# Kernel tuning notes

Measured on AMD Instinct MI355X. Metric: run time of the kernel, lower is better.

The kernel has to match this reference:

```python
import jax, jax.numpy as jnp
import numpy as np

G, KS = 8, 3          # groups, kernel size
K = KS * KS           # sampling points per group
OM = 32               # per-group offset_mask dim: ceil(3K/8)*8
EPS = 1e-5


def setup_inputs() -> dict:
    key = jax.random.key(0)
    ks = jax.random.split(key, 12)
    N, C, H, W = 4, 128, 64, 64
    x = jax.random.normal(ks[0], (N, C, H, W), jnp.float32)
    w_value = jax.random.normal(ks[1], (C, C), jnp.float32) / np.sqrt(C)
    b_value = jax.random.normal(ks[2], (C,), jnp.float32) * 0.01
    # small offset weights -> modest sampling offsets (real module inits these to 0)
    w_off = jax.random.normal(ks[3], (C, G * OM), jnp.float32) * 0.02
    b_off = jax.random.normal(ks[4], (G * OM,), jnp.float32) * 0.01
    w_out = jax.random.normal(ks[5], (C, C), jnp.float32) / np.sqrt(C)
    b_out = jax.random.normal(ks[6], (C,), jnp.float32) * 0.01
    bn_gamma = jax.random.uniform(ks[7], (C,), jnp.float32, 0.5, 1.5)
    bn_beta = jax.random.normal(ks[8], (C,), jnp.float32) * 0.1
    bn_mean = jax.random.normal(ks[9], (C,), jnp.float32) * 0.1
    bn_var = jax.random.uniform(ks[10], (C,), jnp.float32, 0.5, 1.5)
    return dict(x=x, w_value=w_value, b_value=b_value, w_off=w_off, b_off=b_off,
                w_out=w_out, b_out=b_out, bn_gamma=bn_gamma, bn_beta=bn_beta,
                bn_mean=bn_mean, bn_var=bn_var)


def _dcnv4(x, w_value, b_value, w_off, b_off, w_out, b_out,
           bn_gamma, bn_beta, bn_mean, bn_var):
    N, C, H, W = x.shape
    Cg = C // G
    P = H * W
    xf = x.transpose(0, 2, 3, 1).reshape(N, P, C)              # N,P,C (channels-last tokens)
    val = xf @ w_value + b_value                               # value projection
    om = (xf @ w_off + b_off).reshape(N, P, G, OM)             # offsets+mask (padded to 32)
    offset = om[..., :2 * K].reshape(N, P, G, K, 2)            # (dx, dy) pairs
    mask = om[..., 2 * K:3 * K]                                # modulation, NO softmax (DCNv4)

    # base sampling grid: output pixel + centered 3x3 footprint (stride 1, dil 1)
    py, px = jnp.meshgrid(jnp.arange(H), jnp.arange(W), indexing='ij')
    kk = jnp.arange(KS) - (KS - 1) // 2
    ky, kx = jnp.meshgrid(kk, kk, indexing='ij')
    base_y = (py.reshape(-1)[:, None] + ky.reshape(-1)[None, :]).astype(x.dtype)  # P,K
    base_x = (px.reshape(-1)[:, None] + kx.reshape(-1)[None, :]).astype(x.dtype)
    sy = base_y[None, :, None, :] + offset[..., 1]             # N,P,G,K sampling y
    sx = base_x[None, :, None, :] + offset[..., 0]             # N,P,G,K sampling x

    vflat = val.reshape(N, P, G, Cg).transpose(0, 2, 1, 3)     # N,G,P,Cg

    def gather(iy, ix):
        lin = jnp.clip(iy, 0, H - 1) * W + jnp.clip(ix, 0, W - 1)   # N,P,G,K
        lin = lin.transpose(0, 2, 1, 3).reshape(N, G, P * K)
        g = jnp.take_along_axis(vflat, lin[..., None], axis=2)      # N,G,P*K,Cg
        return g.reshape(N, G, P, K, Cg).transpose(0, 2, 1, 3, 4)   # N,P,G,K,Cg

    y0 = jnp.floor(sy); x0 = jnp.floor(sx)
    ty = sy - y0; tx = sx - x0
    y0i = y0.astype(jnp.int32); x0i = x0.astype(jnp.int32)

    def valid(iy, ix):
        return ((iy >= 0) & (iy < H) & (ix >= 0) & (ix < W)).astype(x.dtype)

    acc = jnp.zeros((N, P, G, K, Cg), x.dtype)
    for dy, dx, wgt in ((0, 0, (1 - ty) * (1 - tx)), (0, 1, (1 - ty) * tx),
                        (1, 0, ty * (1 - tx)), (1, 1, ty * tx)):
        iy, ix = y0i + dy, x0i + dx
        acc = acc + gather(iy, ix) * (wgt * valid(iy, ix))[..., None]

    out = (acc * mask[..., None]).sum(axis=3)                  # aggregate over K -> N,P,G,Cg
    out = out.reshape(N, P, C) @ w_out + b_out                 # output projection
    out = out.reshape(N, H, W, C).transpose(0, 3, 1, 2)        # back to NCHW

    # BatchNorm (inference) + SiLU
    inv = bn_gamma / jnp.sqrt(bn_var + EPS)
    out = out * inv[None, :, None, None] + (bn_beta - bn_mean * inv)[None, :, None, None]
    return out * jax.nn.sigmoid(out)


def reference(x, w_value, b_value, w_off, b_off, w_out, b_out,
              bn_gamma, bn_beta, bn_mean, bn_var):
    return _dcnv4(x, w_value, b_value, w_off, b_off, w_out, b_out,
                  bn_gamma, bn_beta, bn_mean, bn_var)
```

## Files before the change

### kernel.cpp

```cpp
#include <hip/hip_runtime.h>
#include <cstdint>

typedef __bf16 v8bf __attribute__((ext_vector_type(8)));
typedef float f32x4 __attribute__((ext_vector_type(4)));

#define BN_EPS 1e-5f

__device__ __forceinline__ float b2f(uint32_t u) {
    union { uint32_t i; float f; } v; v.i = u << 16; return v.f;
}
__device__ __forceinline__ uint16_t f2b(float f) {
    uint32_t u = __builtin_bit_cast(uint32_t, f);
    u += 0x7fffu + ((u >> 16) & 1u);
    return (uint16_t)(u >> 16);
}

__global__ void prep_transpose_kernel(const float* __restrict__ x,
                                      const float* __restrict__ wv, const float* __restrict__ wo,
                                      const float* __restrict__ wout,
                                      const float* __restrict__ gamma, const float* __restrict__ beta,
                                      const float* __restrict__ mean, const float* __restrict__ var,
                                      uint16_t* __restrict__ xf, uint16_t* __restrict__ wT,
                                      float* __restrict__ bnc) {
    int bid = blockIdx.x;
    if (bid < 512) {
        __shared__ float lds[64 * 65];
        int cb = bid & 1, pb = (bid >> 1) & 63, n = bid >> 7;
        int c0 = cb * 64, p0 = pb * 64;
        int l = threadIdx.x & 63, q = threadIdx.x >> 6;
        const float* xp = x + ((size_t)(n * 128 + c0)) * 4096 + p0;
#pragma unroll
        for (int i = 0; i < 16; i++) {
            int c = i * 4 + q;
            lds[l * 65 + c] = xp[(size_t)c * 4096 + l];
        }
        __syncthreads();
#pragma unroll
        for (int i = 0; i < 16; i++) {
            int pr = i * 4 + q;
            xf[((size_t)(n * 4096 + p0 + pr)) * 128 + c0 + l] = f2b(lds[pr * 65 + l]);
        }
    } else {
        int idx = (bid - 512) * 256 + threadIdx.x;
        if (idx < 512 * 128) {
            int r = idx >> 7, ci = idx & 127;
            float v;
            if (r < 128)      v = wv[ci * 128 + r];
            else if (r < 384) v = wo[ci * 256 + (r - 128)];
            else              v = wout[ci * 128 + (r - 384)];
            wT[idx] = f2b(v);
        }
        if (idx < 128) {
            float inv = gamma[idx] * rsqrtf(var[idx] + BN_EPS);
            bnc[idx] = inv;
            bnc[128 + idx] = beta[idx] - mean[idx] * inv;
        }
    }
}

__launch_bounds__(256)
__global__ void gemm1_kernel(const uint16_t* __restrict__ xf, const uint16_t* __restrict__ wT,
                             const float* __restrict__ b_value, const float* __restrict__ b_off,
                             uint16_t* __restrict__ valb, uint16_t* __restrict__ omb) {
    __shared__ __align__(16) uint16_t ldsX[128 * 136];
    __shared__ __align__(16) uint16_t ldsW[64 * 136];
    int ct = blockIdx.x;
    int pt = blockIdx.y;
    int p0 = pt * 128, cbase = ct * 64;
    int tid = threadIdx.x;
    int col16 = tid & 15, rowq = tid >> 4;

    const uint4* xg = (const uint4*)xf;
    uint4* lx = (uint4*)ldsX;
#pragma unroll
    for (int i = 0; i < 8; i++) {
        int row = i * 16 + rowq;
        lx[row * 17 + col16] = xg[(size_t)(p0 + row) * 16 + col16];
    }
    const uint4* wg = (const uint4*)wT;
    uint4* lw = (uint4*)ldsW;
#pragma unroll
    for (int i = 0; i < 4; i++) {
        int row = i * 16 + rowq;
        lw[row * 17 + col16] = wg[(size_t)(cbase + row) * 16 + col16];
    }
    __syncthreads();

    int wv = tid >> 6, lane = tid & 63;
    int ln = lane & 15, quad = lane >> 4;
    int cW = cbase + wv * 16 + quad * 4;
    f32x4 binit;
    if (cW < 128) binit = f32x4{b_value[cW], b_value[cW + 1], b_value[cW + 2], b_value[cW + 3]};
    else          binit = f32x4{b_off[cW - 128], b_off[cW - 127], b_off[cW - 126], b_off[cW - 125]};
    f32x4 acc[8];
#pragma unroll
    for (int t = 0; t < 8; t++) acc[t] = binit;

#pragma unroll
    for (int kk = 0; kk < 4; kk++) {
        v8bf a = *(const v8bf*)&ldsW[(wv * 16 + ln) * 136 + kk * 32 + quad * 8];
#pragma unroll
        for (int t = 0; t < 8; t++) {
            v8bf b = *(const v8bf*)&ldsX[(t * 16 + ln) * 136 + kk * 32 + quad * 8];
            acc[t] = __builtin_amdgcn_mfma_f32_16x16x32_bf16(a, b, acc[t], 0, 0, 0);
        }
    }

    int nimg = p0 >> 12, pin0 = p0 & 4095;
    if (cW < 128) {
        int g = cW >> 4, cg = cW & 15;
#pragma unroll
        for (int t = 0; t < 8; t++) {
            int p = pin0 + t * 16 + ln;
            uint32_t u0 = (uint32_t)f2b(acc[t][0]) | ((uint32_t)f2b(acc[t][1]) << 16);
            uint32_t u1 = (uint32_t)f2b(acc[t][2]) | ((uint32_t)f2b(acc[t][3]) << 16);
            *(uint2*)&valb[(((size_t)(nimg * 8 + g) * 4096 + p) << 4) + cg] = make_uint2(u0, u1);
        }
    } else {
        int j0 = cW - 128;
#pragma unroll
        for (int t = 0; t < 8; t++) {
            int p = pin0 + t * 16 + ln;
            uint32_t u0 = (uint32_t)f2b(acc[t][0]) | ((uint32_t)f2b(acc[t][1]) << 16);
            uint32_t u1 = (uint32_t)f2b(acc[t][2]) | ((uint32_t)f2b(acc[t][3]) << 16);
            *(uint2*)&omb[((size_t)(nimg * 4096 + p) << 8) + j0] = make_uint2(u0, u1);
        }
    }
}

__launch_bounds__(256)
__global__ void gather_gemm3_kernel(const uint16_t* __restrict__ omb, const uint16_t* __restrict__ valb,
                                    const uint16_t* __restrict__ wT,
                                    const float* __restrict__ b_out, const float* __restrict__ bnc,
                                    float* __restrict__ out) {
    __shared__ __align__(16) uint16_t ldsA[64 * 136];
    __shared__ __align__(16) uint16_t ldsW[128 * 136];
    int pt = blockIdx.x;
    int p0 = pt * 64;
    int n = p0 >> 12, pin0 = p0 & 4095;
    int tid = threadIdx.x;

    {
        int col16 = tid & 15, rowq = tid >> 4;
        const uint4* wg = (const uint4*)wT;
        uint4* lw = (uint4*)ldsW;
#pragma unroll
        for (int i = 0; i < 8; i++) {
            int row = i * 16 + rowq;
            lw[row * 17 + col16] = wg[(size_t)(384 + row) * 16 + col16];
        }
    }

    int g = tid >> 5, pl = tid & 31;
    const uint4* vb = (const uint4*)(valb + ((size_t)(n * 8 + g) << 16));
#pragma unroll
    for (int pp = 0; pp < 2; pp++) {
        int prow = pp * 32 + pl;
        int p = p0 + prow;
        int pin = p & 4095;
        int py = pin >> 6, px = pin & 63;

        const uint16_t* op = omb + ((size_t)p << 8) + g * 32;
        uint4 q0 = *(const uint4*)(op);
        uint4 q1 = *(const uint4*)(op + 8);
        uint4 q2 = *(const uint4*)(op + 16);
        uint2 q3 = *(const uint2*)(op + 24);
        uint32_t w[14] = {q0.x, q0.y, q0.z, q0.w, q1.x, q1.y, q1.z, q1.w,
                          q2.x, q2.y, q2.z, q2.w, q3.x, q3.y};
        float o[28];
#pragma unroll
        for (int i = 0; i < 14; i++) { o[2 * i] = b2f(w[i] & 0xffff); o[2 * i + 1] = b2f(w[i] >> 16); }

        float acc[16];
#pragma unroll
        for (int i = 0; i < 16; i++) acc[i] = 0.f;

#pragma unroll
        for (int k = 0; k < 9; k++) {
            float sx = (float)(px + (k % 3) - 1) + o[2 * k];
            float sy = (float)(py + (k / 3) - 1) + o[2 * k + 1];
            float m = o[18 + k];
            float x0f = floorf(sx), y0f = floorf(sy);
            float tx = sx - x0f, ty = sy - y0f;
            int x0 = (int)x0f, y0 = (int)y0f;
#pragma unroll
            for (int dy = 0; dy < 2; dy++) {
                int iy = y0 + dy;
                if (iy < 0 || iy > 63) continue;
                float wy = dy ? ty : 1.f - ty;
#pragma unroll
                for (int dx = 0; dx < 2; dx++) {
                    int ix = x0 + dx;
                    if (ix < 0 || ix > 63) continue;
                    float wgt = m * wy * (dx ? tx : 1.f - tx);
                    const uint4* vp = vb + ((size_t)(iy * 64 + ix)) * 2;
                    uint4 v0 = vp[0], v1 = vp[1];
                    acc[0]  += wgt * b2f(v0.x & 0xffff); acc[1]  += wgt * b2f(v0.x >> 16);
                    acc[2]  += wgt * b2f(v0.y & 0xffff); acc[3]  += wgt * b2f(v0.y >> 16);
                    acc[4]  += wgt * b2f(v0.z & 0xffff); acc[5]  += wgt * b2f(v0.z >> 16);
                    acc[6]  += wgt * b2f(v0.w & 0xffff); acc[7]  += wgt * b2f(v0.w >> 16);
                    acc[8]  += wgt * b2f(v1.x & 0xffff); acc[9]  += wgt * b2f(v1.x >> 16);
                    acc[10] += wgt * b2f(v1.y & 0xffff); acc[11] += wgt * b2f(v1.y >> 16);
                    acc[12] += wgt * b2f(v1.z & 0xffff); acc[13] += wgt * b2f(v1.z >> 16);
                    acc[14] += wgt * b2f(v1.w & 0xffff); acc[15] += wgt * b2f(v1.w >> 16);
                }
            }
        }
        uint32_t u[8];
#pragma unroll
        for (int i = 0; i < 8; i++)
            u[i] = (uint32_t)f2b(acc[2 * i]) | ((uint32_t)f2b(acc[2 * i + 1]) << 16);
        uint4* outp = (uint4*)&ldsA[prow * 136 + g * 16];
        outp[0] = make_uint4(u[0], u[1], u[2], u[3]);
        outp[1] = make_uint4(u[4], u[5], u[6], u[7]);
    }
    __syncthreads();

    int wv = tid >> 6, lane = tid & 63;
    int ln = lane & 15, quad = lane >> 4;
    f32x4 acc[8];
#pragma unroll
    for (int ni = 0; ni < 8; ni++) {
        float b = b_out[ni * 16 + ln];
        acc[ni] = f32x4{b, b, b, b};
    }
#pragma unroll
    for (int kk = 0; kk < 4; kk++) {
        v8bf a = *(const v8bf*)&ldsA[(wv * 16 + ln) * 136 + kk * 32 + quad * 8];
#pragma unroll
        for (int ni = 0; ni < 8; ni++) {
            v8bf b = *(const v8bf*)&ldsW[(ni * 16 + ln) * 136 + kk * 32 + quad * 8];
            acc[ni] = __builtin_amdgcn_mfma_f32_16x16x32_bf16(a, b, acc[ni], 0, 0, 0);
        }
    }
    int p = pin0 + wv * 16 + quad * 4;
#pragma unroll
    for (int ni = 0; ni < 8; ni++) {
        int cc = ni * 16 + ln;
        float inv = bnc[cc], add = bnc[128 + cc];
        float4 r;
        float* rp = &r.x;
#pragma unroll
        for (int q = 0; q < 4; q++) {
            float z = acc[ni][q] * inv + add;
            rp[q] = z / (1.f + __expf(-z));
        }
        *(float4*)&out[((size_t)(n * 128 + cc) << 12) + p] = r;
    }
}

extern "C" void kernel_launch(void* const* d_in, const int* in_sizes, int n_in,
                              void* d_out, int out_size, void* d_ws, size_t ws_size,
                              hipStream_t stream) {
    const float* x       = (const float*)d_in[0];
    const float* w_value = (const float*)d_in[1];
    const float* b_value = (const float*)d_in[2];
    const float* w_off   = (const float*)d_in[3];
    const float* b_off   = (const float*)d_in[4];
    const float* w_out   = (const float*)d_in[5];
    const float* b_out   = (const float*)d_in[6];
    const float* gamma   = (const float*)d_in[7];
    const float* beta    = (const float*)d_in[8];
    const float* mean    = (const float*)d_in[9];
    const float* var     = (const float*)d_in[10];
    float* out = (float*)d_out;

    char* ws = (char*)d_ws;
    uint16_t* xf   = (uint16_t*)(ws);
    uint16_t* valb = (uint16_t*)(ws + ((size_t)8 << 20));
    uint16_t* omb  = (uint16_t*)(ws + ((size_t)12 << 20));
    uint16_t* wT   = (uint16_t*)(ws + ((size_t)20 << 20));
    float*    bnc  = (float*)(ws + ((size_t)20 << 20) + (1 << 18));

    hipLaunchKernelGGL(prep_transpose_kernel, dim3(768), dim3(256), 0, stream,
                       x, w_value, w_off, w_out, gamma, beta, mean, var, xf, wT, bnc);
    hipLaunchKernelGGL(gemm1_kernel, dim3(6, 128), dim3(256), 0, stream,
                       xf, wT, b_value, b_off, valb, omb);
    hipLaunchKernelGGL(gather_gemm3_kernel, dim3(256), dim3(256), 0, stream,
                       omb, valb, wT, b_out, bnc, out);
}
```

Baseline: 118.6 us.

## Split gather across channel halves and shrink gather-GEMM tile to 16 pixels

The gather+output-projection kernel now handles 16 pixels per block instead of 64 and launches 1024 blocks instead of 256. Each thread covers one pixel, one group and half of that group's channels, so each thread loads one 16-byte value vector per bilinear corner instead of two. The GEMM stage is split by output-channel tiles across waves. The BatchNorm constants are now computed inside the epilogue rather than in the prep kernel. The aim is more parallelism and more memory requests in flight in the latency-bound gather, at the cost of reloading the 128x128 weight tile into LDS four times as often and repeating the offset/mask work across the two channel halves.

```diff
diff --git a/kernel.cpp b/kernel.cpp
--- a/kernel.cpp
+++ b/kernel.cpp
@@ -18,10 +18,7 @@
 __global__ void prep_transpose_kernel(const float* __restrict__ x,
                                       const float* __restrict__ wv, const float* __restrict__ wo,
                                       const float* __restrict__ wout,
-                                      const float* __restrict__ gamma, const float* __restrict__ beta,
-                                      const float* __restrict__ mean, const float* __restrict__ var,
-                                      uint16_t* __restrict__ xf, uint16_t* __restrict__ wT,
-                                      float* __restrict__ bnc) {
+                                      uint16_t* __restrict__ xf, uint16_t* __restrict__ wT) {
     int bid = blockIdx.x;
     if (bid < 512) {
         __shared__ float lds[64 * 65];
@@ -49,11 +46,6 @@
             else if (r < 384) v = wo[ci * 256 + (r - 128)];
             else              v = wout[ci * 128 + (r - 384)];
             wT[idx] = f2b(v);
-        }
-        if (idx < 128) {
-            float inv = gamma[idx] * rsqrtf(var[idx] + BN_EPS);
-            bnc[idx] = inv;
-            bnc[128 + idx] = beta[idx] - mean[idx] * inv;
         }
     }
 }
@@ -131,12 +123,14 @@
 __launch_bounds__(256)
 __global__ void gather_gemm3_kernel(const uint16_t* __restrict__ omb, const uint16_t* __restrict__ valb,
                                     const uint16_t* __restrict__ wT,
-                                    const float* __restrict__ b_out, const float* __restrict__ bnc,
+                                    const float* __restrict__ b_out,
+                                    const float* __restrict__ gamma, const float* __restrict__ beta,
+                                    const float* __restrict__ mean, const float* __restrict__ var,
                                     float* __restrict__ out) {
-    __shared__ __align__(16) uint16_t ldsA[64 * 136];
+    __shared__ __align__(16) uint16_t ldsA[16 * 136];
     __shared__ __align__(16) uint16_t ldsW[128 * 136];
     int pt = blockIdx.x;
-    int p0 = pt * 64;
+    int p0 = pt * 16;
     int n = p0 >> 12, pin0 = p0 & 4095;
     int tid = threadIdx.x;
 
@@ -151,101 +145,92 @@
         }
     }
 
-    int g = tid >> 5, pl = tid & 31;
-    const uint4* vb = (const uint4*)(valb + ((size_t)(n * 8 + g) << 16));
-#pragma unroll
-    for (int pp = 0; pp < 2; pp++) {
-        int prow = pp * 32 + pl;
-        int p = p0 + prow;
-        int pin = p & 4095;
-        int py = pin >> 6, px = pin & 63;
-
-        const uint16_t* op = omb + ((size_t)p << 8) + g * 32;
-        uint4 q0 = *(const uint4*)(op);
-        uint4 q1 = *(const uint4*)(op + 8);
-        uint4 q2 = *(const uint4*)(op + 16);
-        uint2 q3 = *(const uint2*)(op + 24);
-        uint32_t w[14] = {q0.x, q0.y, q0.z, q0.w, q1.x, q1.y, q1.z, q1.w,
-                          q2.x, q2.y, q2.z, q2.w, q3.x, q3.y};
-        float o[28];
-#pragma unroll
-        for (int i = 0; i < 14; i++) { o[2 * i] = b2f(w[i] & 0xffff); o[2 * i + 1] = b2f(w[i] >> 16); }
-
-        float acc[16];
-#pragma unroll
-        for (int i = 0; i < 16; i++) acc[i] = 0.f;
-
-#pragma unroll
-        for (int k = 0; k < 9; k++) {
-            float sx = (float)(px + (k % 3) - 1) + o[2 * k];
-            float sy = (float)(py + (k / 3) - 1) + o[2 * k + 1];
-            float m = o[18 + k];
-            float x0f = floorf(sx), y0f = floorf(sy);
-            float tx = sx - x0f, ty = sy - y0f;
-            int x0 = (int)x0f, y0 = (int)y0f;
-#pragma unroll
-            for (int dy = 0; dy < 2; dy++) {
-                int iy = y0 + dy;
-                if (iy < 0 || iy > 63) continue;
-                float wy = dy ? ty : 1.f - ty;
-#pragma unroll
-                for (int dx = 0; dx < 2; dx++) {
-                    int ix = x0 + dx;
-                    if (ix < 0 || ix > 63) continue;
-                    float wgt = m * wy * (dx ? tx : 1.f - tx);
-                    const uint4* vp = vb + ((size_t)(iy * 64 + ix)) * 2;
-                    uint4 v0 = vp[0], v1 = vp[1];
-                    acc[0]  += wgt * b2f(v0.x & 0xffff); acc[1]  += wgt * b2f(v0.x >> 16);
-                    acc[2]  += wgt * b2f(v0.y & 0xffff); acc[3]  += wgt * b2f(v0.y >> 16);
-                    acc[4]  += wgt * b2f(v0.z & 0xffff); acc[5]  += wgt * b2f(v0.z >> 16);
-                    acc[6]  += wgt * b2f(v0.w & 0xffff); acc[7]  += wgt * b2f(v0.w >> 16);
-                    acc[8]  += wgt * b2f(v1.x & 0xffff); acc[9]  += wgt * b2f(v1.x >> 16);
-                    acc[10] += wgt * b2f(v1.y & 0xffff); acc[11] += wgt * b2f(v1.y >> 16);
-                    acc[12] += wgt * b2f(v1.z & 0xffff); acc[13] += wgt * b2f(v1.z >> 16);
-                    acc[14] += wgt * b2f(v1.w & 0xffff); acc[15] += wgt * b2f(v1.w >> 16);
-                }
+    int pl = tid & 15, g = (tid >> 4) & 7, h = tid >> 7;
+    int p = p0 + pl;
+    int pin = p & 4095;
+    int py = pin >> 6, px = pin & 63;
+
+    const uint16_t* op = omb + ((size_t)p << 8) + g * 32;
+    uint4 q0 = *(const uint4*)(op);
+    uint4 q1 = *(const uint4*)(op + 8);
+    uint4 q2 = *(const uint4*)(op + 16);
+    uint2 q3 = *(const uint2*)(op + 24);
+    uint32_t w[14] = {q0.x, q0.y, q0.z, q0.w, q1.x, q1.y, q1.z, q1.w,
+                      q2.x, q2.y, q2.z, q2.w, q3.x, q3.y};
+    float o[28];
+#pragma unroll
+    for (int i = 0; i < 14; i++) { o[2 * i] = b2f(w[i] & 0xffff); o[2 * i + 1] = b2f(w[i] >> 16); }
+
+    float acc[8];
+#pragma unroll
+    for (int i = 0; i < 8; i++) acc[i] = 0.f;
+
+    const uint4* vb = (const uint4*)(valb + ((size_t)(n * 8 + g) << 16)) + h;
+#pragma unroll
+    for (int k = 0; k < 9; k++) {
+        float sx = (float)(px + (k % 3) - 1) + o[2 * k];
+        float sy = (float)(py + (k / 3) - 1) + o[2 * k + 1];
+        float m = o[18 + k];
+        float x0f = floorf(sx), y0f = floorf(sy);
+        float tx = sx - x0f, ty = sy - y0f;
+        int x0 = (int)x0f, y0 = (int)y0f;
+        float wy[2] = {m * (1.f - ty), m * ty};
+        float wx[2] = {1.f - tx, tx};
+#pragma unroll
+        for (int dy = 0; dy < 2; dy++) {
+            int iy = y0 + dy;
+            if (iy < 0 || iy > 63) continue;
+#pragma unroll
+            for (int dx = 0; dx < 2; dx++) {
+                int ix = x0 + dx;
+                if (ix < 0 || ix > 63) continue;
+                float wgt = wy[dy] * wx[dx];
+                uint4 v0 = vb[((size_t)(iy * 64 + ix)) * 2];
+                acc[0] += wgt * b2f(v0.x & 0xffff); acc[1] += wgt * b2f(v0.x >> 16);
+                acc[2] += wgt * b2f(v0.y & 0xffff); acc[3] += wgt * b2f(v0.y >> 16);
+                acc[4] += wgt * b2f(v0.z & 0xffff); acc[5] += wgt * b2f(v0.z >> 16);
+                acc[6] += wgt * b2f(v0.w & 0xffff); acc[7] += wgt * b2f(v0.w >> 16);
             }
         }
-        uint32_t u[8];
-#pragma unroll
-        for (int i = 0; i < 8; i++)
-            u[i] = (uint32_t)f2b(acc[2 * i]) | ((uint32_t)f2b(acc[2 * i + 1]) << 16);
-        uint4* outp = (uint4*)&ldsA[prow * 136 + g * 16];
-        outp[0] = make_uint4(u[0], u[1], u[2], u[3]);
-        outp[1] = make_uint4(u[4], u[5], u[6], u[7]);
-    }
+    }
+    uint32_t u[4];
+#pragma unroll
+    for (int i = 0; i < 4; i++)
+        u[i] = (uint32_t)f2b(acc[2 * i]) | ((uint32_t)f2b(acc[2 * i + 1]) << 16);
+    *(uint4*)&ldsA[pl * 136 + g * 16 + h * 8] = make_uint4(u[0], u[1], u[2], u[3]);
     __syncthreads();
 
     int wv = tid >> 6, lane = tid & 63;
     int ln = lane & 15, quad = lane >> 4;
-    f32x4 acc[8];
-#pragma unroll
-    for (int ni = 0; ni < 8; ni++) {
-        float b = b_out[ni * 16 + ln];
-        acc[ni] = f32x4{b, b, b, b};
+    f32x4 acc2[2];
+#pragma unroll
+    for (int t = 0; t < 2; t++) {
+        float b = b_out[(wv * 2 + t) * 16 + ln];
+        acc2[t] = f32x4{b, b, b, b};
     }
 #pragma unroll
     for (int kk = 0; kk < 4; kk++) {
-        v8bf a = *(const v8bf*)&ldsA[(wv * 16 + ln) * 136 + kk * 32 + quad * 8];
-#pragma unroll
-        for (int ni = 0; ni < 8; ni++) {
-            v8bf b = *(const v8bf*)&ldsW[(ni * 16 + ln) * 136 + kk * 32 + quad * 8];
-            acc[ni] = __builtin_amdgcn_mfma_f32_16x16x32_bf16(a, b, acc[ni], 0, 0, 0);
-        }
-    }
-    int p = pin0 + wv * 16 + quad * 4;
-#pragma unroll
-    for (int ni = 0; ni < 8; ni++) {
-        int cc = ni * 16 + ln;
-        float inv = bnc[cc], add = bnc[128 + cc];
+        v8bf a = *(const v8bf*)&ldsA[ln * 136 + kk * 32 + quad * 8];
+#pragma unroll
+        for (int t = 0; t < 2; t++) {
+            v8bf b = *(const v8bf*)&ldsW[((wv * 2 + t) * 16 + ln) * 136 + kk * 32 + quad * 8];
+            acc2[t] = __builtin_amdgcn_mfma_f32_16x16x32_bf16(a, b, acc2[t], 0, 0, 0);
+        }
+    }
+    int pp = pin0 + quad * 4;
+#pragma unroll
+    for (int t = 0; t < 2; t++) {
+        int cc = (wv * 2 + t) * 16 + ln;
+        float inv = gamma[cc] * __frsqrt_rn(var[cc] + BN_EPS);
+        float add = beta[cc] - mean[cc] * inv;
         float4 r;
         float* rp = &r.x;
 #pragma unroll
         for (int q = 0; q < 4; q++) {
-            float z = acc[ni][q] * inv + add;
+            float z = acc2[t][q] * inv + add;
             rp[q] = z / (1.f + __expf(-z));
         }
-        *(float4*)&out[((size_t)(n * 128 + cc) << 12) + p] = r;
+        *(float4*)&out[((size_t)(n * 128 + cc) << 12) + pp] = r;
     }
 }
 
@@ -270,12 +255,11 @@
     uint16_t* valb = (uint16_t*)(ws + ((size_t)8 << 20));
     uint16_t* omb  = (uint16_t*)(ws + ((size_t)12 << 20));
     uint16_t* wT   = (uint16_t*)(ws + ((size_t)20 << 20));
-    float*    bnc  = (float*)(ws + ((size_t)20 << 20) + (1 << 18));
 
     hipLaunchKernelGGL(prep_transpose_kernel, dim3(768), dim3(256), 0, stream,
-                       x, w_value, w_off, w_out, gamma, beta, mean, var, xf, wT, bnc);
+                       x, w_value, w_off, w_out, xf, wT);
     hipLaunchKernelGGL(gemm1_kernel, dim3(6, 128), dim3(256), 0, stream,
                        xf, wT, b_value, b_off, valb, omb);
-    hipLaunchKernelGGL(gather_gemm3_kernel, dim3(256), dim3(256), 0, stream,
-                       omb, valb, wT, b_out, bnc, out);
-}
+    hipLaunchKernelGGL(gather_gemm3_kernel, dim3(1024), dim3(256), 0, stream,
+                       omb, valb, wT, b_out, gamma, beta, mean, var, out);
+}
```

New measurement: 112.4 us. 5.2% less time.
